# Kernel optimization log

Measured on AMD Instinct MI355X. Metric: run time of the kernel, lower is better.

Reference implementation:

```python
import jax, jax.numpy as jnp
import numpy as np

N = 50000      # nodes
E = 1600000    # edges (avg degree 32)
D_IN = 128
HID = 64


def setup_inputs() -> dict:
    key = jax.random.key(0)
    ks = jax.random.split(key, 7)
    x = jax.random.normal(ks[0], (N, D_IN), dtype=jnp.float32)
    ei = jax.random.randint(ks[1], (2, E), 0, N, dtype=jnp.int32)
    ew = jax.random.uniform(ks[2], (E,), dtype=jnp.float32)
    # GCNConv linear weights (glorot-ish scale); lin has no bias, conv bias added post-aggregation
    W1 = jax.random.normal(ks[3], (HID, D_IN), dtype=jnp.float32) * (1.0 / np.sqrt(D_IN))
    b1 = jnp.zeros((HID,), dtype=jnp.float32)
    W2 = jax.random.normal(ks[4], (HID, HID), dtype=jnp.float32) * (1.0 / np.sqrt(HID))
    b2 = jnp.zeros((HID,), dtype=jnp.float32)
    return {"x": x, "ei": ei, "ew": ew, "W1": W1, "b1": b1, "W2": W2, "b2": b2}


def _gcn_conv(x, src, dst, ew_all, W, b, n_nodes):
    """PyG GCNConv: gcn_norm (self-loops already appended) + x@W.T, gather-scale-scatter, +b."""
    deg = jax.ops.segment_sum(ew_all, dst, num_segments=n_nodes)  # dst-side weighted degree
    dinv = jnp.where(deg > 0, jax.lax.rsqrt(deg), 0.0)            # deg^{-1/2}, inf->0
    norm = dinv[src] * ew_all * dinv[dst]                          # [E+N]
    h = x @ W.T                                                    # [N, hid]
    msg = h[src] * norm[:, None]                                   # gather + scale
    out = jax.ops.segment_sum(msg, dst, num_segments=n_nodes)     # scatter-add
    return out + b


def reference(x, ei, ew, W1, b1, W2, b2):
    n_nodes = x.shape[0]
    # add self loops once (fill value 1.0), shared by both conv layers
    loop = jnp.arange(n_nodes, dtype=ei.dtype)
    src = jnp.concatenate([ei[0], loop])
    dst = jnp.concatenate([ei[1], loop])
    ew_all = jnp.concatenate([ew, jnp.ones((n_nodes,), dtype=ew.dtype)])

    h1 = jax.nn.relu(_gcn_conv(x, src, dst, ew_all, W1, b1, n_nodes))
    # dropout is identity in eval mode
    h2 = _gcn_conv(h1, src, dst, ew_all, W2, b2, n_nodes)
    return h2 + h1
```

## Files before the change

kernel.cpp:

```cpp
#include <hip/hip_runtime.h>

#define HID 64
#define DIN 128
#define NBLK 512

typedef unsigned long long ull;
typedef unsigned short u16;

static __device__ __forceinline__ u16 f2bf(float f) {
  unsigned u = __float_as_uint(f);
  unsigned lsb = (u >> 16) & 1u;
  u += 0x7fffu + lsb;
  return (u16)(u >> 16);
}


__global__ __launch_bounds__(512) void k_histA(const int* __restrict__ dst,
                                               int* __restrict__ G,
                                               int E, int NBC, int chunk) {
  __shared__ int h[256];
  int b = blockIdx.x, tid = threadIdx.x;
  if (tid < 256) h[tid] = 0;
  __syncthreads();
  int e0 = b * chunk, e1 = min(E, e0 + chunk);
  for (int e = e0 + tid; e < e1; e += 512) atomicAdd(&h[dst[e] >> 8], 1);
  __syncthreads();
  if (tid < NBC) G[tid * NBLK + b] = h[tid];
}


__global__ __launch_bounds__(256) void k_chunksum(const int* __restrict__ G, int* bsum, int L) {
  int b = blockIdx.x, t = threadIdx.x;
  int base = b * 2048;
  int s = 0;
  for (int i = t; i < 2048; i += 256) {
    int g = base + i;
    s += (g < L) ? G[g] : 0;
  }
  __shared__ int red[4];
  for (int o = 32; o > 0; o >>= 1) s += __shfl_down(s, o);
  if ((t & 63) == 0) red[t >> 6] = s;
  __syncthreads();
  if (t == 0) bsum[b] = red[0] + red[1] + red[2] + red[3];
}

__global__ __launch_bounds__(64) void k_scanbsum(int* bsum, int nb) {
  int lane = threadIdx.x;
  int v = (lane < nb) ? bsum[lane] : 0;
  int incl = v;
  for (int o = 1; o < 64; o <<= 1) {
    int u = __shfl_up(incl, o);
    if (lane >= o) incl += u;
  }
  if (lane < nb) bsum[lane] = incl - v;
}

__global__ __launch_bounds__(256) void k_scanfinal(int* G, const int* __restrict__ bsum, int L) {
  int b = blockIdx.x, t = threadIdx.x;
  int i0 = b * 2048 + t * 8;
  int v[8], tsum = 0;
#pragma unroll
  for (int k = 0; k < 8; ++k) {
    v[k] = (i0 + k < L) ? G[i0 + k] : 0;
    tsum += v[k];
  }
  int incl = tsum;
  for (int o = 1; o < 64; o <<= 1) {
    int u = __shfl_up(incl, o);
    if ((t & 63) >= o) incl += u;
  }
  int wexcl = incl - tsum;
  __shared__ int wtot[4];
  int w = t >> 6;
  if ((t & 63) == 63) wtot[w] = incl;
  __syncthreads();
  int wbase = 0;
  for (int i = 0; i < w; ++i) wbase += wtot[i];
  int run = bsum[b] + wbase + wexcl;
#pragma unroll
  for (int k = 0; k < 8; ++k) {
    if (i0 + k < L) G[i0 + k] = run;
    run += v[k];
  }
}


__global__ __launch_bounds__(512) void k_scatterA(const int* __restrict__ src,
                                                  const int* __restrict__ dst,
                                                  const float* __restrict__ ew,
                                                  const int* __restrict__ Gs,
                                                  int2* __restrict__ bufA,
                                                  int E, int NBC, int chunk) {
  __shared__ int cur[256];
  int b = blockIdx.x, tid = threadIdx.x;
  if (tid < NBC) cur[tid] = Gs[tid * NBLK + b];
  __syncthreads();
  int e0 = b * chunk, e1 = min(E, e0 + chunk);
  for (int e = e0 + tid; e < e1; e += 512) {
    int s = src[e], d = dst[e];
    float w = ew[e];
    int p = atomicAdd(&cur[d >> 8], 1);
    bufA[p] = make_int2(__float_as_int(w), (int)(((unsigned)s << 16) | (unsigned)d));
  }
}


__global__ __launch_bounds__(512) void k_passB(const int2* __restrict__ bufA,
                                               const int* __restrict__ Gs,
                                               int2* __restrict__ bufB,
                                               int* __restrict__ offs,
                                               float* __restrict__ dinv,
                                               int NBC, int E, int N) {
  int bin = blockIdx.x, tid = threadIdx.x;
  __shared__ int h2[256];
  __shared__ int cur[256];
  __shared__ float dg[256];
  int base = Gs[bin * NBLK];
  int end  = (bin + 1 < NBC) ? Gs[(bin + 1) * NBLK] : E;
  int m = end - base;
  if (tid < 256) { h2[tid] = 0; dg[tid] = 0.f; }
  __syncthreads();
  for (int i = tid; i < m; i += 512) {
    unsigned sd = (unsigned)bufA[base + i].y;
    atomicAdd(&h2[sd & 255], 1);
  }
  __syncthreads();
  int own = (tid < 256) ? h2[tid] : 0;
  for (int o = 1; o < 256; o <<= 1) {
    int u = 0;
    if (tid < 256 && tid >= o) u = h2[tid - o];
    __syncthreads();
    if (tid < 256) h2[tid] += u;
    __syncthreads();
  }
  int nd = (bin << 8) + tid;
  if (tid < 256) {
    int excl = h2[tid] - own;
    cur[tid] = excl;
    if (nd < N) offs[nd] = base + excl;
  }
  if (bin == NBC - 1 && tid == 0) offs[N] = E;
  __syncthreads();
  for (int i = tid; i < m; i += 512) {
    int2 r = bufA[base + i];
    unsigned sd = (unsigned)r.y;
    int dl = (int)(sd & 255u);
    int p = atomicAdd(&cur[dl], 1);
    bufB[base + p] = r;
    atomicAdd(&dg[dl], __int_as_float(r.x));
  }
  __syncthreads();
  if (tid < 256 && nd < N) dinv[nd] = rsqrtf(1.0f + dg[tid]);
}


__global__ __launch_bounds__(256) void k_norm(int2* __restrict__ recs,
                                              const float* __restrict__ dinv, int E) {
  int e = blockIdx.x * 256 + threadIdx.x;
  if (e < E) {
    int2 r = recs[e];
    unsigned sd = (unsigned)r.y;
    int s = (int)(sd >> 16), d = (int)(sd & 0xffffu);
    float nrm = dinv[s] * __int_as_float(r.x) * dinv[d];
    recs[e] = make_int2(__float_as_int(nrm), s);
  }
}


__global__ __launch_bounds__(256) void k_transW(const float* __restrict__ W,
                                                float* __restrict__ WT, int K) {
  int idx = blockIdx.x * 256 + threadIdx.x;
  if (idx < K * 64) {
    int d = idx >> 6, j = idx & 63;
    WT[idx] = W[j * K + d];
  }
}


template <int K>
__global__ __launch_bounds__(256) void k_gemm(const float* __restrict__ X,
                                              const float* __restrict__ WTg,
                                              u16* __restrict__ out, int n_nodes) {
  constexpr int PAD = 68;
  __shared__ float XT[64 * PAD];
  __shared__ float WL[64 * PAD];
  const int tid = threadIdx.x;
  const int n0 = blockIdx.x * 64;
  const int tx = tid & 15;
  const int ty = tid >> 4;
  float acc[4][4] = {{0.f}};

  for (int ph = 0; ph < K / 64; ++ph) {
    const int d0 = ph * 64;
    __syncthreads();
#pragma unroll
    for (int k = 0; k < 4; ++k) {
      int f = tid + k * 256;
      int r = f >> 4, q = f & 15;
      int n = n0 + r;
      float4 xv = (n < n_nodes)
        ? *reinterpret_cast<const float4*>(&X[(size_t)n * K + d0 + 4 * q])
        : make_float4(0.f, 0.f, 0.f, 0.f);
      *reinterpret_cast<float4*>(&XT[r * PAD + 4 * q]) = xv;
      float4 wv = *reinterpret_cast<const float4*>(&WTg[(size_t)(d0 + r) * 64 + 4 * q]);
      *reinterpret_cast<float4*>(&WL[r * PAD + 4 * q]) = wv;
    }
    __syncthreads();
#pragma unroll 4
    for (int dd = 0; dd < 64; dd += 4) {
      float4 xs[4], ws[4];
#pragma unroll
      for (int mi = 0; mi < 4; ++mi)
        xs[mi] = *reinterpret_cast<const float4*>(&XT[(4 * ty + mi) * PAD + dd]);
#pragma unroll
      for (int dk = 0; dk < 4; ++dk)
        ws[dk] = *reinterpret_cast<const float4*>(&WL[(dd + dk) * PAD + 4 * tx]);
#pragma unroll
      for (int mi = 0; mi < 4; ++mi) {
        float xm[4] = {xs[mi].x, xs[mi].y, xs[mi].z, xs[mi].w};
#pragma unroll
        for (int dk = 0; dk < 4; ++dk) {
          acc[mi][0] = fmaf(xm[dk], ws[dk].x, acc[mi][0]);
          acc[mi][1] = fmaf(xm[dk], ws[dk].y, acc[mi][1]);
          acc[mi][2] = fmaf(xm[dk], ws[dk].z, acc[mi][2]);
          acc[mi][3] = fmaf(xm[dk], ws[dk].w, acc[mi][3]);
        }
      }
    }
  }

#pragma unroll
  for (int mi = 0; mi < 4; ++mi) {
    int n = n0 + 4 * ty + mi;
    if (n < n_nodes) {
      ushort4 o = make_ushort4(f2bf(acc[mi][0]), f2bf(acc[mi][1]),
                               f2bf(acc[mi][2]), f2bf(acc[mi][3]));
      *reinterpret_cast<ushort4*>(&out[(size_t)n * HID + 4 * tx]) = o;
    }
  }
}


__device__ __forceinline__ void bfma(uint2 v, float w,
                                     float& a0, float& a1, float& a2, float& a3) {
  a0 = fmaf(__uint_as_float(v.x << 16), w, a0);
  a1 = fmaf(__uint_as_float(v.x & 0xffff0000u), w, a1);
  a2 = fmaf(__uint_as_float(v.y << 16), w, a2);
  a3 = fmaf(__uint_as_float(v.y & 0xffff0000u), w, a3);
}

__global__ __launch_bounds__(256) void k_agg(const u16* __restrict__ h,
                                             const int2* __restrict__ recs,
                                             const int* __restrict__ offs,
                                             const float* __restrict__ dinv,
                                             const float* __restrict__ bias,
                                             const float* __restrict__ resid,
                                             float* __restrict__ out, int n_nodes, int mode) {
  int gw = __builtin_amdgcn_readfirstlane((int)((blockIdx.x * 256 + threadIdx.x) >> 6));
  if (gw >= n_nodes) return;
  int lane = threadIdx.x & 63;
  int g = lane >> 4;
  int p4 = (lane & 15) * 4;
  int beg = __builtin_amdgcn_readfirstlane(offs[gw]);
  int end = __builtin_amdgcn_readfirstlane(offs[gw + 1]);
  float di = dinv[gw];

  float a0 = 0.f, a1 = 0.f, a2 = 0.f, a3 = 0.f;
  float b0 = 0.f, b1 = 0.f, b2 = 0.f, b3 = 0.f;

  {
    uint2 v = *reinterpret_cast<const uint2*>(&h[(size_t)gw * HID + p4]);
    bfma(v, (g == 0) ? di * di : 0.f, a0, a1, a2, a3);
  }

  int i = beg;
  for (; i + 32 <= end; i += 32) {
    int2 r0 = recs[i + g];       int2 r1 = recs[i + 4 + g];
    int2 r2 = recs[i + 8 + g];   int2 r3 = recs[i + 12 + g];
    int2 r4 = recs[i + 16 + g];  int2 r5 = recs[i + 20 + g];
    int2 r6 = recs[i + 24 + g];  int2 r7 = recs[i + 28 + g];
    uint2 v0 = *reinterpret_cast<const uint2*>(&h[(size_t)r0.y * HID + p4]);
    uint2 v1 = *reinterpret_cast<const uint2*>(&h[(size_t)r1.y * HID + p4]);
    uint2 v2 = *reinterpret_cast<const uint2*>(&h[(size_t)r2.y * HID + p4]);
    uint2 v3 = *reinterpret_cast<const uint2*>(&h[(size_t)r3.y * HID + p4]);
    uint2 v4 = *reinterpret_cast<const uint2*>(&h[(size_t)r4.y * HID + p4]);
    uint2 v5 = *reinterpret_cast<const uint2*>(&h[(size_t)r5.y * HID + p4]);
    uint2 v6 = *reinterpret_cast<const uint2*>(&h[(size_t)r6.y * HID + p4]);
    uint2 v7 = *reinterpret_cast<const uint2*>(&h[(size_t)r7.y * HID + p4]);
    bfma(v0, __int_as_float(r0.x), a0, a1, a2, a3);
    bfma(v1, __int_as_float(r1.x), b0, b1, b2, b3);
    bfma(v2, __int_as_float(r2.x), a0, a1, a2, a3);
    bfma(v3, __int_as_float(r3.x), b0, b1, b2, b3);
    bfma(v4, __int_as_float(r4.x), a0, a1, a2, a3);
    bfma(v5, __int_as_float(r5.x), b0, b1, b2, b3);
    bfma(v6, __int_as_float(r6.x), a0, a1, a2, a3);
    bfma(v7, __int_as_float(r7.x), b0, b1, b2, b3);
  }
  if (i + 16 <= end) {
    int2 r0 = recs[i + g];       int2 r1 = recs[i + 4 + g];
    int2 r2 = recs[i + 8 + g];   int2 r3 = recs[i + 12 + g];
    uint2 v0 = *reinterpret_cast<const uint2*>(&h[(size_t)r0.y * HID + p4]);
    uint2 v1 = *reinterpret_cast<const uint2*>(&h[(size_t)r1.y * HID + p4]);
    uint2 v2 = *reinterpret_cast<const uint2*>(&h[(size_t)r2.y * HID + p4]);
    uint2 v3 = *reinterpret_cast<const uint2*>(&h[(size_t)r3.y * HID + p4]);
    bfma(v0, __int_as_float(r0.x), a0, a1, a2, a3);
    bfma(v1, __int_as_float(r1.x), b0, b1, b2, b3);
    bfma(v2, __int_as_float(r2.x), a0, a1, a2, a3);
    bfma(v3, __int_as_float(r3.x), b0, b1, b2, b3);
    i += 16;
  }
  if (i + 8 <= end) {
    int2 r0 = recs[i + g];       int2 r1 = recs[i + 4 + g];
    uint2 v0 = *reinterpret_cast<const uint2*>(&h[(size_t)r0.y * HID + p4]);
    uint2 v1 = *reinterpret_cast<const uint2*>(&h[(size_t)r1.y * HID + p4]);
    bfma(v0, __int_as_float(r0.x), a0, a1, a2, a3);
    bfma(v1, __int_as_float(r1.x), b0, b1, b2, b3);
    i += 8;
  }
  if (i + 4 <= end) {
    int2 r0 = recs[i + g];
    uint2 v0 = *reinterpret_cast<const uint2*>(&h[(size_t)r0.y * HID + p4]);
    bfma(v0, __int_as_float(r0.x), a0, a1, a2, a3);
    i += 4;
  }
  if (i < end) {
    int rem = end - i;
    int idx = i + ((g < rem) ? g : (rem - 1));
    int2 r = recs[idx];
    float w = (g < rem) ? __int_as_float(r.x) : 0.f;
    uint2 v = *reinterpret_cast<const uint2*>(&h[(size_t)r.y * HID + p4]);
    bfma(v, w, b0, b1, b2, b3);
  }

  float r0 = a0 + b0, r1 = a1 + b1, r2 = a2 + b2, r3 = a3 + b3;
  r0 += __shfl_xor(r0, 16); r0 += __shfl_xor(r0, 32);
  r1 += __shfl_xor(r1, 16); r1 += __shfl_xor(r1, 32);
  r2 += __shfl_xor(r2, 16); r2 += __shfl_xor(r2, 32);
  r3 += __shfl_xor(r3, 16); r3 += __shfl_xor(r3, 32);

  if (g == 0) {
    float4 bb = *reinterpret_cast<const float4*>(&bias[p4]);
    r0 += bb.x; r1 += bb.y; r2 += bb.z; r3 += bb.w;
    if (mode == 0) {
      r0 = fmaxf(r0, 0.f); r1 = fmaxf(r1, 0.f);
      r2 = fmaxf(r2, 0.f); r3 = fmaxf(r3, 0.f);
    } else {
      float4 rs = *reinterpret_cast<const float4*>(&resid[(size_t)gw * HID + p4]);
      r0 += rs.x; r1 += rs.y; r2 += rs.z; r3 += rs.w;
    }
    *reinterpret_cast<float4*>(&out[(size_t)gw * HID + p4]) = make_float4(r0, r1, r2, r3);
  }
}


extern "C" void kernel_launch(void* const* d_in, const int* in_sizes, int n_in,
                              void* d_out, int out_size, void* d_ws, size_t ws_size,
                              hipStream_t stream) {
  const float* x  = (const float*)d_in[0];
  const int*   ei = (const int*)d_in[1];
  const float* ew = (const float*)d_in[2];
  const float* W1 = (const float*)d_in[3];
  const float* b1 = (const float*)d_in[4];
  const float* W2 = (const float*)d_in[5];
  const float* b2 = (const float*)d_in[6];
  float* out = (float*)d_out;

  const int N = in_sizes[0] / DIN;
  const int E = in_sizes[2];
  const int* src = ei;
  const int* dst = ei + E;

  const int NBC = (N + 255) >> 8;
  const int L = NBC * NBLK;
  const int chunk = (E + NBLK - 1) / NBLK;
  const int nch = (L + 2047) / 2048;

  char* p = (char*)d_ws;
  auto carve = [&](size_t bytes) {
    char* r = p;
    p += (bytes + 255) & ~(size_t)255;
    return r;
  };
  int*   G     = (int*)carve((size_t)L * 4);
  int*   bsum  = (int*)carve(64 * 4);
  int*   offs  = (int*)carve((size_t)(N + 1) * 4);
  float* dinv  = (float*)carve((size_t)N * 4);
  int2*  bufA  = (int2*)carve((size_t)E * 8);
  int2*  bufB  = (int2*)carve((size_t)E * 8);
  u16*   h     = (u16*)carve((size_t)N * HID * 2);
  float* h1    = (float*)carve((size_t)N * HID * 4);
  float* WT1   = (float*)carve((size_t)DIN * HID * 4);
  float* WT2   = (float*)carve((size_t)HID * HID * 4);

  int gblk = (N + 63) / 64;
  int ablk = (N + 3) / 4;

  k_histA<<<NBLK, 512, 0, stream>>>(dst, G, E, NBC, chunk);
  k_transW<<<(DIN * HID + 255) / 256, 256, 0, stream>>>(W1, WT1, DIN);
  k_transW<<<(HID * HID + 255) / 256, 256, 0, stream>>>(W2, WT2, HID);
  k_chunksum<<<nch, 256, 0, stream>>>(G, bsum, L);
  k_scanbsum<<<1, 64, 0, stream>>>(bsum, nch);
  k_scanfinal<<<nch, 256, 0, stream>>>(G, bsum, L);
  k_scatterA<<<NBLK, 512, 0, stream>>>(src, dst, ew, G, bufA, E, NBC, chunk);
  k_passB<<<NBC, 512, 0, stream>>>(bufA, G, bufB, offs, dinv, NBC, E, N);
  k_norm<<<(E + 255) / 256, 256, 0, stream>>>(bufB, dinv, E);

  k_gemm<DIN><<<gblk, 256, 0, stream>>>(x, WT1, h, N);
  k_agg<<<ablk, 256, 0, stream>>>(h, bufB, offs, dinv, b1, nullptr, h1, N, 0);
  k_gemm<HID><<<gblk, 256, 0, stream>>>(h1, WT2, h, N);
  k_agg<<<ablk, 256, 0, stream>>>(h, bufB, offs, dinv, b2, h1, out, N, 1);
}
```

Measured before the change: 244.6 us.

## Assign one node per 16-lane quarter-wave in aggregation, fuse weight transposes

The aggregation kernel now maps four nodes per wavefront, one per 16-lane group, instead of one node per wave split four ways over edges. This removes the cross-group shuffle reduction and the masked tail handling, and launches four times fewer blocks. In exchange, loops diverge within a wave when the four nodes have different degrees, and each group's edge-record loads are no longer spread across lanes. The two weight-transpose launches are also merged into one kernel.

```diff
diff --git a/kernel.cpp b/kernel.cpp
--- a/kernel.cpp
+++ b/kernel.cpp
@@ -167,12 +167,19 @@
 }
 
 
-__global__ __launch_bounds__(256) void k_transW(const float* __restrict__ W,
-                                                float* __restrict__ WT, int K) {
+__global__ __launch_bounds__(256) void k_transW2(const float* __restrict__ W1,
+                                                 const float* __restrict__ W2,
+                                                 float* __restrict__ WT1,
+                                                 float* __restrict__ WT2) {
   int idx = blockIdx.x * 256 + threadIdx.x;
-  if (idx < K * 64) {
+  if (idx < DIN * 64) {
     int d = idx >> 6, j = idx & 63;
-    WT[idx] = W[j * K + d];
+    WT1[idx] = W1[j * DIN + d];
+  }
+  int i2 = idx - DIN * 64;
+  if (i2 >= 0 && i2 < HID * 64) {
+    int d = i2 >> 6, j = i2 & 63;
+    WT2[i2] = W2[j * HID + d];
   }
 }
 
@@ -256,29 +263,32 @@
                                              const float* __restrict__ bias,
                                              const float* __restrict__ resid,
                                              float* __restrict__ out, int n_nodes, int mode) {
-  int gw = __builtin_amdgcn_readfirstlane((int)((blockIdx.x * 256 + threadIdx.x) >> 6));
-  if (gw >= n_nodes) return;
-  int lane = threadIdx.x & 63;
-  int g = lane >> 4;
+  int tid = threadIdx.x;
+  int lane = tid & 63;
+  int q = lane >> 4;
   int p4 = (lane & 15) * 4;
-  int beg = __builtin_amdgcn_readfirstlane(offs[gw]);
-  int end = __builtin_amdgcn_readfirstlane(offs[gw + 1]);
-  float di = dinv[gw];
-
-  float a0 = 0.f, a1 = 0.f, a2 = 0.f, a3 = 0.f;
+  int node = (blockIdx.x * 4 + (tid >> 6)) * 4 + q;
+  if (node >= n_nodes) return;
+  int beg = offs[node], end = offs[node + 1];
+  float di = dinv[node];
+
+  float a0, a1, a2, a3;
   float b0 = 0.f, b1 = 0.f, b2 = 0.f, b3 = 0.f;
-
   {
-    uint2 v = *reinterpret_cast<const uint2*>(&h[(size_t)gw * HID + p4]);
-    bfma(v, (g == 0) ? di * di : 0.f, a0, a1, a2, a3);
+    uint2 v = *reinterpret_cast<const uint2*>(&h[(size_t)node * HID + p4]);
+    float w = di * di;
+    a0 = __uint_as_float(v.x << 16) * w;
+    a1 = __uint_as_float(v.x & 0xffff0000u) * w;
+    a2 = __uint_as_float(v.y << 16) * w;
+    a3 = __uint_as_float(v.y & 0xffff0000u) * w;
   }
 
   int i = beg;
-  for (; i + 32 <= end; i += 32) {
-    int2 r0 = recs[i + g];       int2 r1 = recs[i + 4 + g];
-    int2 r2 = recs[i + 8 + g];   int2 r3 = recs[i + 12 + g];
-    int2 r4 = recs[i + 16 + g];  int2 r5 = recs[i + 20 + g];
-    int2 r6 = recs[i + 24 + g];  int2 r7 = recs[i + 28 + g];
+  while (i + 8 <= end) {
+    int2 r0 = recs[i];     int2 r1 = recs[i + 1];
+    int2 r2 = recs[i + 2]; int2 r3 = recs[i + 3];
+    int2 r4 = recs[i + 4]; int2 r5 = recs[i + 5];
+    int2 r6 = recs[i + 6]; int2 r7 = recs[i + 7];
     uint2 v0 = *reinterpret_cast<const uint2*>(&h[(size_t)r0.y * HID + p4]);
     uint2 v1 = *reinterpret_cast<const uint2*>(&h[(size_t)r1.y * HID + p4]);
     uint2 v2 = *reinterpret_cast<const uint2*>(&h[(size_t)r2.y * HID + p4]);
@@ -295,10 +305,11 @@
     bfma(v5, __int_as_float(r5.x), b0, b1, b2, b3);
     bfma(v6, __int_as_float(r6.x), a0, a1, a2, a3);
     bfma(v7, __int_as_float(r7.x), b0, b1, b2, b3);
-  }
-  if (i + 16 <= end) {
-    int2 r0 = recs[i + g];       int2 r1 = recs[i + 4 + g];
-    int2 r2 = recs[i + 8 + g];   int2 r3 = recs[i + 12 + g];
+    i += 8;
+  }
+  if (i + 4 <= end) {
+    int2 r0 = recs[i];     int2 r1 = recs[i + 1];
+    int2 r2 = recs[i + 2]; int2 r3 = recs[i + 3];
     uint2 v0 = *reinterpret_cast<const uint2*>(&h[(size_t)r0.y * HID + p4]);
     uint2 v1 = *reinterpret_cast<const uint2*>(&h[(size_t)r1.y * HID + p4]);
     uint2 v2 = *reinterpret_cast<const uint2*>(&h[(size_t)r2.y * HID + p4]);
@@ -307,49 +318,33 @@
     bfma(v1, __int_as_float(r1.x), b0, b1, b2, b3);
     bfma(v2, __int_as_float(r2.x), a0, a1, a2, a3);
     bfma(v3, __int_as_float(r3.x), b0, b1, b2, b3);
-    i += 16;
-  }
-  if (i + 8 <= end) {
-    int2 r0 = recs[i + g];       int2 r1 = recs[i + 4 + g];
+    i += 4;
+  }
+  if (i + 2 <= end) {
+    int2 r0 = recs[i];     int2 r1 = recs[i + 1];
     uint2 v0 = *reinterpret_cast<const uint2*>(&h[(size_t)r0.y * HID + p4]);
     uint2 v1 = *reinterpret_cast<const uint2*>(&h[(size_t)r1.y * HID + p4]);
     bfma(v0, __int_as_float(r0.x), a0, a1, a2, a3);
     bfma(v1, __int_as_float(r1.x), b0, b1, b2, b3);
-    i += 8;
-  }
-  if (i + 4 <= end) {
-    int2 r0 = recs[i + g];
+    i += 2;
+  }
+  if (i < end) {
+    int2 r0 = recs[i];
     uint2 v0 = *reinterpret_cast<const uint2*>(&h[(size_t)r0.y * HID + p4]);
     bfma(v0, __int_as_float(r0.x), a0, a1, a2, a3);
-    i += 4;
-  }
-  if (i < end) {
-    int rem = end - i;
-    int idx = i + ((g < rem) ? g : (rem - 1));
-    int2 r = recs[idx];
-    float w = (g < rem) ? __int_as_float(r.x) : 0.f;
-    uint2 v = *reinterpret_cast<const uint2*>(&h[(size_t)r.y * HID + p4]);
-    bfma(v, w, b0, b1, b2, b3);
   }
 
   float r0 = a0 + b0, r1 = a1 + b1, r2 = a2 + b2, r3 = a3 + b3;
-  r0 += __shfl_xor(r0, 16); r0 += __shfl_xor(r0, 32);
-  r1 += __shfl_xor(r1, 16); r1 += __shfl_xor(r1, 32);
-  r2 += __shfl_xor(r2, 16); r2 += __shfl_xor(r2, 32);
-  r3 += __shfl_xor(r3, 16); r3 += __shfl_xor(r3, 32);
-
-  if (g == 0) {
-    float4 bb = *reinterpret_cast<const float4*>(&bias[p4]);
-    r0 += bb.x; r1 += bb.y; r2 += bb.z; r3 += bb.w;
-    if (mode == 0) {
-      r0 = fmaxf(r0, 0.f); r1 = fmaxf(r1, 0.f);
-      r2 = fmaxf(r2, 0.f); r3 = fmaxf(r3, 0.f);
-    } else {
-      float4 rs = *reinterpret_cast<const float4*>(&resid[(size_t)gw * HID + p4]);
-      r0 += rs.x; r1 += rs.y; r2 += rs.z; r3 += rs.w;
-    }
-    *reinterpret_cast<float4*>(&out[(size_t)gw * HID + p4]) = make_float4(r0, r1, r2, r3);
-  }
+  float4 bb = *reinterpret_cast<const float4*>(&bias[p4]);
+  r0 += bb.x; r1 += bb.y; r2 += bb.z; r3 += bb.w;
+  if (mode == 0) {
+    r0 = fmaxf(r0, 0.f); r1 = fmaxf(r1, 0.f);
+    r2 = fmaxf(r2, 0.f); r3 = fmaxf(r3, 0.f);
+  } else {
+    float4 rs = *reinterpret_cast<const float4*>(&resid[(size_t)node * HID + p4]);
+    r0 += rs.x; r1 += rs.y; r2 += rs.z; r3 += rs.w;
+  }
+  *reinterpret_cast<float4*>(&out[(size_t)node * HID + p4]) = make_float4(r0, r1, r2, r3);
 }
 
 
@@ -393,11 +388,10 @@
   float* WT2   = (float*)carve((size_t)HID * HID * 4);
 
   int gblk = (N + 63) / 64;
-  int ablk = (N + 3) / 4;
+  int ablk = (N + 15) / 16;
 
   k_histA<<<NBLK, 512, 0, stream>>>(dst, G, E, NBC, chunk);
-  k_transW<<<(DIN * HID + 255) / 256, 256, 0, stream>>>(W1, WT1, DIN);
-  k_transW<<<(HID * HID + 255) / 256, 256, 0, stream>>>(W2, WT2, HID);
+  k_transW2<<<((DIN + HID) * 64 + 255) / 256, 256, 0, stream>>>(W1, W2, WT1, WT2);
   k_chunksum<<<nch, 256, 0, stream>>>(G, bsum, L);
   k_scanbsum<<<1, 64, 0, stream>>>(bsum, nch);
   k_scanfinal<<<nch, 256, 0, stream>>>(G, bsum, L);
```

Result: faster. 233.1 us (-4.7%).
